# Kernel tuning notes

Hardware: AMD Instinct MI355X
Metric: run time of the kernel (lower is better)

## Reference

```python
import jax, jax.numpy as jnp
import numpy as np

B, S, D_MODEL, H = 2, 2048, 1024, 16
DK = D_MODEL // H
THETA = 10000.0


def setup_inputs() -> dict:
    key = jax.random.key(0)
    ks = jax.random.split(key, 5)
    scale = 0.02  # keep logits in a numerically sane range
    return {
        "x": jax.random.normal(ks[0], (B, S, D_MODEL), jnp.float32),
        "Q_weight": jax.random.normal(ks[1], (D_MODEL, D_MODEL), jnp.float32) * scale,
        "K_weight": jax.random.normal(ks[2], (D_MODEL, D_MODEL), jnp.float32) * scale,
        "V_weight": jax.random.normal(ks[3], (D_MODEL, D_MODEL), jnp.float32) * scale,
        "O_weight": jax.random.normal(ks[4], (D_MODEL, D_MODEL), jnp.float32) * scale,
        "token_positions": jnp.arange(S, dtype=jnp.int32),
    }


def _rope(x, token_positions, theta, d_k):
    # x: [..., seq, d_k]; rotate interleaved even/odd pairs
    inv_freq = 1.0 / theta ** (jnp.arange(0, d_k, 2, dtype=jnp.float32) / d_k)
    ang = token_positions.astype(jnp.float32)[:, None] * inv_freq  # [S, d_k/2]
    cos, sin = jnp.cos(ang), jnp.sin(ang)
    x0, x1 = x[..., 0::2], x[..., 1::2]
    y0 = x0 * cos - x1 * sin
    y1 = x0 * sin + x1 * cos
    return jnp.stack([y0, y1], axis=-1).reshape(x.shape)


def _mhsa(x, Qw, Kw, Vw, Ow, token_positions):
    b, s, d = x.shape
    qw = Qw.reshape(H, DK, d)
    kw = Kw.reshape(H, DK, d)
    vw = Vw.reshape(H, DK, d)
    q = jnp.einsum('hki,bsi->bhsk', qw, x)
    k = jnp.einsum('hki,bsi->bhsk', kw, x)
    v = jnp.einsum('hvi,bsi->bhsv', vw, x)
    q = _rope(q, token_positions, THETA, DK)
    k = _rope(k, token_positions, THETA, DK)
    scores = jnp.einsum('bhnd,bhmd->bhnm', q, k) / jnp.sqrt(jnp.float32(DK))
    causal = jnp.tril(jnp.ones((s, s), dtype=bool))
    scores = jnp.where(causal, scores, -jnp.inf)
    attn = jax.nn.softmax(scores, axis=-1)
    o = jnp.einsum('bhnm,bhmv->bhnv', attn, v)  # [B,H,S,DV]
    o = jnp.transpose(o, (0, 2, 1, 3)).reshape(b, s, H * DK)
    return jnp.einsum('dv,bsv->bsd', Ow, o)


def reference(x, Q_weight, K_weight, V_weight, O_weight, token_positions):
    return _mhsa(x, Q_weight, K_weight, V_weight, O_weight, token_positions)
```

## Files before the change

kernel.cpp:

```cpp
#include <hip/hip_runtime.h>

#define NB 2
#define NS 2048
#define NDM 1024
#define NH 16
#define NDK 64

typedef unsigned int u32;
typedef u32 u32x4 __attribute__((ext_vector_type(4)));
typedef float f32x4 __attribute__((ext_vector_type(4)));
typedef float f32x2 __attribute__((ext_vector_type(2)));
typedef __bf16 bf16x8 __attribute__((ext_vector_type(8)));
typedef __bf16 bf16x4 __attribute__((ext_vector_type(4)));
typedef __bf16 bf16x2 __attribute__((ext_vector_type(2)));

#define QSCALE 0.18033688011112042f
#define EXP2F(x) __builtin_amdgcn_exp2f(x)

__device__ __forceinline__ void gload_lds16(const __bf16* g, __bf16* l) {
    __builtin_amdgcn_global_load_lds(
        (const __attribute__((address_space(1))) unsigned int*)(g),
        (__attribute__((address_space(3))) unsigned int*)(l), 16, 0, 0);
}

__global__ __launch_bounds__(256) void cvt_f32_bf16(const float* __restrict__ src,
                                                    __bf16* __restrict__ dst, int n4) {
    int i = blockIdx.x * blockDim.x + threadIdx.x;
    if (i >= n4) return;
    f32x4 v = *(const f32x4*)(src + (size_t)i * 4);
    bf16x4 o;
    o[0] = (__bf16)v[0]; o[1] = (__bf16)v[1]; o[2] = (__bf16)v[2]; o[3] = (__bf16)v[3];
    *(bf16x4*)(dst + (size_t)i * 4) = o;
}

__global__ __launch_bounds__(256) void cvt_weights(const float* __restrict__ q,
                                                   const float* __restrict__ k,
                                                   const float* __restrict__ v,
                                                   const float* __restrict__ o,
                                                   __bf16* __restrict__ wqkv,
                                                   __bf16* __restrict__ owb) {
    const int seg = blockIdx.y;
    const float* src = (seg == 0) ? q : (seg == 1) ? k : (seg == 2) ? v : o;
    __bf16* dst = (seg == 3) ? owb : wqkv + (size_t)seg * 1024 * 1024;
    const int i = blockIdx.x * 256 + threadIdx.x;
    f32x4 vv = *(const f32x4*)(src + (size_t)i * 4);
    bf16x4 ov;
    ov[0] = (__bf16)vv[0]; ov[1] = (__bf16)vv[1]; ov[2] = (__bf16)vv[2]; ov[3] = (__bf16)vv[3];
    *(bf16x4*)(dst + (size_t)i * 4) = ov;
}

__global__ __launch_bounds__(512, 2) void gemm256(const __bf16* __restrict__ A,
                                                  const __bf16* __restrict__ Bt,
                                                  __bf16* __restrict__ C,
                                                  int K, int lda, int ldb, int ldc, int nbx) {
    __shared__ __bf16 As[2][256 * 64];
    __shared__ __bf16 Bs[2][256 * 64];
    const int tid = threadIdx.x;
    const int lane = tid & 63, w = tid >> 6;
    const int wm = w >> 2, wn = w & 3;
    const int l15 = lane & 15, lg = lane >> 4;
    int bid = blockIdx.x;
    const int cpx = gridDim.x >> 3;
    bid = (bid & 7) * cpx + (bid >> 3);
    const int m0 = (bid / nbx) * 256, n0 = (bid % nbx) * 256;
    const int srow = w * 8 + (lane >> 3);
    const int csw = ((lane & 7) ^ (srow & 7)) * 8;

    f32x4 acc[8][4];
    const f32x4 z = {0.f, 0.f, 0.f, 0.f};
#pragma unroll
    for (int i = 0; i < 8; ++i)
#pragma unroll
        for (int jx = 0; jx < 4; ++jx) acc[i][jx] = z;

    auto stage = [&](int buf, int k0) {
#pragma unroll
        for (int ps = 0; ps < 4; ++ps) {
            const int r = ps * 64 + srow;
            gload_lds16(&A[(size_t)(m0 + r) * lda + k0 + csw], &As[buf][(ps * 64 + w * 8) * 64]);
        }
#pragma unroll
        for (int ps = 0; ps < 4; ++ps) {
            const int r = ps * 64 + srow;
            gload_lds16(&Bt[(size_t)(n0 + r) * ldb + k0 + csw], &Bs[buf][(ps * 64 + w * 8) * 64]);
        }
    };

    stage(0, 0);
    int cur = 0;
    for (int k0 = 0; k0 < K; k0 += 64) {
        if (k0 + 64 < K) {
            stage(cur ^ 1, k0 + 64);
            asm volatile("s_waitcnt vmcnt(8)" ::: "memory");
        } else {
            asm volatile("s_waitcnt vmcnt(0)" ::: "memory");
        }
        __builtin_amdgcn_s_barrier();
        __builtin_amdgcn_sched_barrier(0);
        bf16x8 bfr[4][2];
#pragma unroll
        for (int n = 0; n < 4; ++n)
#pragma unroll
            for (int kc = 0; kc < 2; ++kc) {
                const int rb = wn * 64 + n * 16 + l15;
                bfr[n][kc] = *(const bf16x8*)&Bs[cur][rb * 64 + ((kc * 32 + lg * 8) ^ ((rb & 7) << 3))];
            }
#pragma unroll
        for (int mr = 0; mr < 8; ++mr) {
            bf16x8 af[2];
#pragma unroll
            for (int kc = 0; kc < 2; ++kc) {
                const int ra = wm * 128 + mr * 16 + l15;
                af[kc] = *(const bf16x8*)&As[cur][ra * 64 + ((kc * 32 + lg * 8) ^ ((ra & 7) << 3))];
            }
#pragma unroll
            for (int n = 0; n < 4; ++n)
#pragma unroll
                for (int kc = 0; kc < 2; ++kc)
                    acc[mr][n] = __builtin_amdgcn_mfma_f32_16x16x32_bf16(af[kc], bfr[n][kc], acc[mr][n], 0, 0, 0);
        }
        asm volatile("s_waitcnt lgkmcnt(0)" ::: "memory");
        __builtin_amdgcn_s_barrier();
        __builtin_amdgcn_sched_barrier(0);
        cur ^= 1;
    }
#pragma unroll
    for (int mr = 0; mr < 8; ++mr)
#pragma unroll
        for (int n = 0; n < 4; ++n)
#pragma unroll
            for (int j = 0; j < 4; ++j) {
                const int row = m0 + wm * 128 + mr * 16 + lg * 4 + j;
                const int col = n0 + wn * 64 + n * 16 + l15;
                C[(size_t)row * ldc + col] = (__bf16)acc[mr][n][j];
            }
}

template <typename TOUT>
__global__ __launch_bounds__(256) void gemm_bt128(const __bf16* __restrict__ A,
                                                  const __bf16* __restrict__ Bt,
                                                  TOUT* __restrict__ C,
                                                  int K, int lda, int ldb, int ldc) {
    __shared__ __bf16 As[2][128 * 64];
    __shared__ __bf16 Bs[2][128 * 64];
    const int tid = threadIdx.x;
    const int lane = tid & 63, w = tid >> 6;
    const int wr = w >> 1, wc = w & 1;
    const int l15 = lane & 15, lg = lane >> 4;
    const int m0 = blockIdx.y * 128, n0 = blockIdx.x * 128;
    const int crow = lane >> 3;
    const int csw = ((lane & 7) ^ crow) * 8;

    f32x4 acc[4][4];
    const f32x4 z = {0.f, 0.f, 0.f, 0.f};
#pragma unroll
    for (int i = 0; i < 4; ++i)
#pragma unroll
        for (int jx = 0; jx < 4; ++jx) acc[i][jx] = z;

    auto stage = [&](int buf, int k0) {
#pragma unroll
        for (int ch = 0; ch < 4; ++ch) {
            const int cid = w * 4 + ch;
            const int ra = cid * 8 + crow;
            gload_lds16(&A[(size_t)(m0 + ra) * lda + k0 + csw], &As[buf][cid * 512]);
            gload_lds16(&Bt[(size_t)(n0 + ra) * ldb + k0 + csw], &Bs[buf][cid * 512]);
        }
    };

    stage(0, 0);
    int cur = 0;
    for (int k0 = 0; k0 < K; k0 += 64) {
        if (k0 + 64 < K) {
            stage(cur ^ 1, k0 + 64);
            asm volatile("s_waitcnt vmcnt(8)" ::: "memory");
        } else {
            asm volatile("s_waitcnt vmcnt(0)" ::: "memory");
        }
        __builtin_amdgcn_s_barrier();
        __builtin_amdgcn_sched_barrier(0);
#pragma unroll
        for (int kc = 0; kc < 2; ++kc) {
            bf16x8 af[4], bfv[4];
#pragma unroll
            for (int i = 0; i < 4; ++i) {
                const int ra = wr * 64 + i * 16 + l15;
                const int rb = wc * 64 + i * 16 + l15;
                af[i]  = *(const bf16x8*)&As[cur][ra * 64 + ((kc * 32 + lg * 8) ^ ((ra & 7) << 3))];
                bfv[i] = *(const bf16x8*)&Bs[cur][rb * 64 + ((kc * 32 + lg * 8) ^ ((rb & 7) << 3))];
            }
#pragma unroll
            for (int sm = 0; sm < 4; ++sm)
#pragma unroll
                for (int sn = 0; sn < 4; ++sn)
                    acc[sm][sn] = __builtin_amdgcn_mfma_f32_16x16x32_bf16(af[sm], bfv[sn], acc[sm][sn], 0, 0, 0);
        }
        asm volatile("s_waitcnt lgkmcnt(0)" ::: "memory");
        __builtin_amdgcn_s_barrier();
        __builtin_amdgcn_sched_barrier(0);
        cur ^= 1;
    }
#pragma unroll
    for (int sm = 0; sm < 4; ++sm)
#pragma unroll
        for (int sn = 0; sn < 4; ++sn)
#pragma unroll
            for (int j = 0; j < 4; ++j) {
                const int row = m0 + wr * 64 + sm * 16 + lg * 4 + j;
                const int col = n0 + wc * 64 + sn * 16 + l15;
                C[(size_t)row * ldc + col] = (TOUT)acc[sm][sn][j];
            }
}

__global__ __launch_bounds__(512) void rope_kernel(const __bf16* __restrict__ qkv,
                                                   const int* __restrict__ tp,
                                                   __bf16* __restrict__ Qr,
                                                   __bf16* __restrict__ Kr) {
    const int row = blockIdx.x;
    const int s = row & (NS - 1);
    const int b = row >> 11;
    const int t = threadIdx.x;
    const int h = t >> 5, jj = t & 31;
    const float pos = (float)tp[s];
    const float inv = exp2f(-0.41524101186092f * (float)jj);
    const float ang = pos * inv;
    float sn, cs;
    sincosf(ang, &sn, &cs);
    const __bf16* qp = qkv + (size_t)row * 3072 + h * 64 + 2 * jj;
    bf16x2 qv = *(const bf16x2*)qp;
    bf16x2 kv = *(const bf16x2*)(qp + 1024);
    const float q0 = (float)qv[0], q1 = (float)qv[1];
    const float k0 = (float)kv[0], k1 = (float)kv[1];
    const size_t o = ((size_t)(b * NH + h) * NS + s) * 64 + 2 * jj;
    bf16x2 qo, ko;
    qo[0] = (__bf16)((q0 * cs - q1 * sn) * QSCALE);
    qo[1] = (__bf16)((q0 * sn + q1 * cs) * QSCALE);
    ko[0] = (__bf16)(k0 * cs - k1 * sn); ko[1] = (__bf16)(k0 * sn + k1 * cs);
    *(bf16x2*)&Qr[o] = qo;
    *(bf16x2*)&Kr[o] = ko;
}

__global__ __launch_bounds__(256) void vtrans(const __bf16* __restrict__ qkv,
                                              __bf16* __restrict__ Vt) {
    const int bh = blockIdx.y;
    const int s0 = blockIdx.x * 64;
    const int b = bh >> 4, h = bh & 15;
    __shared__ __bf16 tile[64][72];
    const int t = threadIdx.x;
    const int sl = t >> 3, c8 = (t & 7) * 8;
#pragma unroll
    for (int pp = 0; pp < 2; ++pp) {
        const int srow = sl + pp * 32;
        bf16x8 v = *(const bf16x8*)&qkv[(size_t)(b * NS + s0 + srow) * 3072 + 2048 + h * 64 + c8];
        *(bf16x8*)&tile[srow][c8] = v;
    }
    __syncthreads();
    const int d = t >> 2;
#pragma unroll
    for (int pp = 0; pp < 2; ++pp) {
        const int vec = (t & 3) + pp * 4;
        bf16x8 o;
#pragma unroll
        for (int i = 0; i < 8; ++i) o[i] = tile[vec * 8 + i][d];
        *(bf16x8*)&Vt[((size_t)bh * 64 + d) * NS + s0 + vec * 8] = o;
    }
}

__device__ __forceinline__ int kperm(int rt) {
    const int ct = rt >> 4, rr = rt & 15;
    return ((rr >> 2) << 3) + ((ct >> 1) << 5) + ((ct & 1) << 2) + (rr & 3);
}

__global__ __launch_bounds__(256) void attn5(const __bf16* __restrict__ Qr,
                                             const __bf16* __restrict__ Kr,
                                             const __bf16* __restrict__ Vt,
                                             __bf16* __restrict__ O) {
    const int lid = blockIdx.x;
    const int xcd = lid & 7, ix = lid >> 3;
    const int bh = xcd * 4 + (ix & 3);
    const int p  = ix >> 2;
    const int b = bh >> 4, h = bh & 15;
    const int tid = threadIdx.x;
    const int w = tid >> 6, lane = tid & 63;
    const int l15 = lane & 15, lg = lane >> 4;
    const __bf16* Qb = Qr + (size_t)bh * NS * 64;
    const __bf16* Kb = Kr + (size_t)bh * NS * 64;
    const __bf16* Vb = Vt + (size_t)bh * 64 * NS;

    __shared__ __bf16 Ks[2][64 * 64];
    __shared__ __bf16 Vs[2][64 * 64];

    const int rbv[2] = {p * 64 + w * 16, (31 - p) * 64 + w * 16};

    bf16x8 qf[2][2];
#pragma unroll
    for (int rs = 0; rs < 2; ++rs)
#pragma unroll
        for (int kc = 0; kc < 2; ++kc)
            qf[rs][kc] = *(const bf16x8*)(Qb + (size_t)(rbv[rs] + l15) * 64 + kc * 32 + lg * 8);

    f32x4 oacc[2][4];
    const f32x4 z = {0.f, 0.f, 0.f, 0.f};
#pragma unroll
    for (int rs = 0; rs < 2; ++rs)
#pragma unroll
        for (int ct = 0; ct < 4; ++ct) oacc[rs][ct] = z;
    float m[2], lsum[2];
#pragma unroll
    for (int rs = 0; rs < 2; ++rs) { m[rs] = -1e30f; lsum[rs] = 0.f; }

    const int crow = lane >> 3;
    const int cswz = ((lane & 7) ^ crow) * 8;

#pragma unroll
    for (int pp = 0; pp < 2; ++pp) {
        const int ch = w + pp * 4;
        const int rt = ch * 8 + crow;
        gload_lds16(Kb + (size_t)kperm(rt) * 64 + cswz, &Ks[0][ch * 512]);
        gload_lds16(Vb + (size_t)rt * NS + 0 + cswz, &Vs[0][ch * 512]);
    }
    __syncthreads();

    const int nt = 32 - p;
    for (int t = 0; t < nt; ++t) {
        const int cur = t & 1;
        const int kv0 = t << 6;
        if (t + 1 < nt) {
            const int kv1 = kv0 + 64;
#pragma unroll
            for (int pp = 0; pp < 2; ++pp) {
                const int ch = w + pp * 4;
                const int rt = ch * 8 + crow;
                gload_lds16(Kb + (size_t)(kv1 + kperm(rt)) * 64 + cswz, &Ks[cur ^ 1][ch * 512]);
                gload_lds16(Vb + (size_t)rt * NS + kv1 + cswz, &Vs[cur ^ 1][ch * 512]);
            }
        }
        bool act[2];
        act[0] = (kv0 <= rbv[0] + 15);
        act[1] = true;
        f32x4 sc[2][4];
#pragma unroll
        for (int rs = 0; rs < 2; ++rs)
            if (act[rs])
#pragma unroll
                for (int ct = 0; ct < 4; ++ct) sc[rs][ct] = z;
#pragma unroll
        for (int kc = 0; kc < 2; ++kc) {
            bf16x8 kf[4];
#pragma unroll
            for (int ct = 0; ct < 4; ++ct) {
                const int rt = ct * 16 + l15;
                kf[ct] = *(const bf16x8*)&Ks[cur][rt * 64 + ((kc * 32 + lg * 8) ^ ((rt & 7) << 3))];
            }
#pragma unroll
            for (int rs = 0; rs < 2; ++rs)
                if (act[rs])
#pragma unroll
                    for (int ct = 0; ct < 4; ++ct)
                        sc[rs][ct] = __builtin_amdgcn_mfma_f32_16x16x32_bf16(kf[ct], qf[rs][kc], sc[rs][ct], 0, 0, 0);
        }
        bf16x8 pb[2][2];
#pragma unroll
        for (int rs = 0; rs < 2; ++rs) {
            if (!act[rs]) continue;
            const int rbase = rbv[rs];
            const int qrow = rbase + l15;
            const bool needmask = (kv0 + 63 > rbase);
            if (needmask) {
#pragma unroll
                for (int ct = 0; ct < 4; ++ct)
#pragma unroll
                    for (int j = 0; j < 4; ++j) {
                        const int kvg = kv0 + ((ct >> 1) << 5) + lg * 8 + ((ct & 1) << 2) + j;
                        if (kvg > qrow) sc[rs][ct][j] = -1e30f;
                    }
            }
            float t0 = fmaxf(fmaxf(sc[rs][0][0], sc[rs][0][1]), fmaxf(sc[rs][0][2], sc[rs][0][3]));
            float t1 = fmaxf(fmaxf(sc[rs][1][0], sc[rs][1][1]), fmaxf(sc[rs][1][2], sc[rs][1][3]));
            float t2 = fmaxf(fmaxf(sc[rs][2][0], sc[rs][2][1]), fmaxf(sc[rs][2][2], sc[rs][2][3]));
            float t3 = fmaxf(fmaxf(sc[rs][3][0], sc[rs][3][1]), fmaxf(sc[rs][3][2], sc[rs][3][3]));
            float mt = fmaxf(fmaxf(t0, t1), fmaxf(t2, t3));
            mt = fmaxf(mt, __shfl_xor(mt, 16, 64));
            mt = fmaxf(mt, __shfl_xor(mt, 32, 64));
            float alpha = 1.0f;
            if (!__all(mt - m[rs] <= 12.0f)) {
                const float mn = fmaxf(m[rs], mt);
                alpha = EXP2F(m[rs] - mn);
                m[rs] = mn;
#pragma unroll
                for (int ct = 0; ct < 4; ++ct)
#pragma unroll
                    for (int j = 0; j < 4; ++j) oacc[rs][ct][j] *= alpha;
            }
            float ps = 0.f;
#pragma unroll
            for (int ct = 0; ct < 4; ++ct)
#pragma unroll
                for (int j = 0; j < 4; ++j) {
                    const float e = EXP2F(sc[rs][ct][j] - m[rs]);
                    sc[rs][ct][j] = e;
                    ps += e;
                }
            ps += __shfl_xor(ps, 16, 64);
            ps += __shfl_xor(ps, 32, 64);
            lsum[rs] = lsum[rs] * alpha + ps;
#pragma unroll
            for (int kc = 0; kc < 2; ++kc) {
                bf16x8 pk;
                pk[0] = (__bf16)sc[rs][2 * kc][0];     pk[1] = (__bf16)sc[rs][2 * kc][1];
                pk[2] = (__bf16)sc[rs][2 * kc][2];     pk[3] = (__bf16)sc[rs][2 * kc][3];
                pk[4] = (__bf16)sc[rs][2 * kc + 1][0]; pk[5] = (__bf16)sc[rs][2 * kc + 1][1];
                pk[6] = (__bf16)sc[rs][2 * kc + 1][2]; pk[7] = (__bf16)sc[rs][2 * kc + 1][3];
                pb[rs][kc] = pk;
            }
        }
#pragma unroll
        for (int kc = 0; kc < 2; ++kc) {
            bf16x8 vf[4];
#pragma unroll
            for (int ct = 0; ct < 4; ++ct) {
                const int rt = ct * 16 + l15;
                vf[ct] = *(const bf16x8*)&Vs[cur][rt * 64 + ((kc * 32 + lg * 8) ^ ((rt & 7) << 3))];
            }
#pragma unroll
            for (int rs = 0; rs < 2; ++rs) {
                if (!act[rs]) continue;
#pragma unroll
                for (int ct = 0; ct < 4; ++ct)
                    oacc[rs][ct] = __builtin_amdgcn_mfma_f32_16x16x32_bf16(vf[ct], pb[rs][kc], oacc[rs][ct], 0, 0, 0);
            }
        }
        __syncthreads();
    }
#pragma unroll
    for (int rs = 0; rs < 2; ++rs) {
        const float rl = 1.0f / lsum[rs];
        const size_t rowoff = (size_t)(b * NS + rbv[rs] + l15) * NDM + h * 64 + lg * 4;
#pragma unroll
        for (int ct = 0; ct < 4; ++ct) {
            bf16x4 ov;
#pragma unroll
            for (int j = 0; j < 4; ++j) ov[j] = (__bf16)(oacc[rs][ct][j] * rl);
            *(bf16x4*)&O[rowoff + ct * 16] = ov;
        }
    }
}

extern "C" void kernel_launch(void* const* d_in, const int* in_sizes, int n_in,
                              void* d_out, int out_size, void* d_ws, size_t ws_size,
                              hipStream_t stream) {
    const float* x  = (const float*)d_in[0];
    const float* Qw = (const float*)d_in[1];
    const float* Kw = (const float*)d_in[2];
    const float* Vw = (const float*)d_in[3];
    const float* Ow = (const float*)d_in[4];
    const int*   tp = (const int*)d_in[5];
    float* out = (float*)d_out;

    char* ws = (char*)d_ws;
    size_t off = 0;
    auto alloc = [&](size_t bytes) -> void* {
        void* p = ws + off;
        off += (bytes + 255) & ~(size_t)255;
        return p;
    };
    __bf16* xb   = (__bf16*)alloc((size_t)4096 * 1024 * 2);
    __bf16* wqkv = (__bf16*)alloc((size_t)3072 * 1024 * 2);
    __bf16* owb  = (__bf16*)alloc((size_t)1024 * 1024 * 2);
    __bf16* qkv  = (__bf16*)alloc((size_t)4096 * 3072 * 2);
    __bf16* qr   = (__bf16*)alloc((size_t)32 * 2048 * 64 * 2);
    __bf16* kr   = (__bf16*)alloc((size_t)32 * 2048 * 64 * 2);
    __bf16* vt   = (__bf16*)alloc((size_t)32 * 64 * 2048 * 2);
    __bf16* ob   = (__bf16*)alloc((size_t)4096 * 1024 * 2);

    cvt_f32_bf16<<<4096, 256, 0, stream>>>(x, xb, 4096 * 1024 / 4);
    cvt_weights<<<dim3(1024, 4), 256, 0, stream>>>(Qw, Kw, Vw, Ow, wqkv, owb);

    gemm256<<<192, 512, 0, stream>>>(xb, wqkv, qkv, 1024, 1024, 1024, 3072, 12);
    rope_kernel<<<4096, 512, 0, stream>>>(qkv, tp, qr, kr);
    vtrans<<<dim3(NS / 64, NB * NH), 256, 0, stream>>>(qkv, vt);
    attn5<<<dim3(512), 256, 0, stream>>>(qr, kr, vt, ob);
    gemm_bt128<float><<<dim3(1024 / 128, 4096 / 128), 256, 0, stream>>>(
        ob, owb, out, 1024, 1024, 1024, 1024);
}
```

Measured before the change: 124.9 us.

## Precompute RoPE cos/sin table and use finer waitcnt barriers in attention loop

```diff
diff --git a/kernel.cpp b/kernel.cpp
--- a/kernel.cpp
+++ b/kernel.cpp
@@ -47,6 +47,20 @@
     bf16x4 ov;
     ov[0] = (__bf16)vv[0]; ov[1] = (__bf16)vv[1]; ov[2] = (__bf16)vv[2]; ov[3] = (__bf16)vv[3];
     *(bf16x4*)(dst + (size_t)i * 4) = ov;
+}
+
+__global__ __launch_bounds__(256) void rope_table(const int* __restrict__ tp,
+                                                  float* __restrict__ tbl) {
+    const int i = blockIdx.x * 256 + threadIdx.x;
+    if (i >= NS * 32) return;
+    const int s = i >> 5, jj = i & 31;
+    const float pos = (float)tp[s];
+    const float inv = exp2f(-0.41524101186092f * (float)jj);
+    const float ang = pos * inv;
+    float sn, cs;
+    sincosf(ang, &sn, &cs);
+    f32x2 o; o[0] = cs; o[1] = sn;
+    *(f32x2*)&tbl[(size_t)i * 2] = o;
 }
 
 __global__ __launch_bounds__(512, 2) void gemm256(const __bf16* __restrict__ A,
@@ -213,7 +227,7 @@
 }
 
 __global__ __launch_bounds__(512) void rope_kernel(const __bf16* __restrict__ qkv,
-                                                   const int* __restrict__ tp,
+                                                   const float* __restrict__ tbl,
                                                    __bf16* __restrict__ Qr,
                                                    __bf16* __restrict__ Kr) {
     const int row = blockIdx.x;
@@ -221,11 +235,8 @@
     const int b = row >> 11;
     const int t = threadIdx.x;
     const int h = t >> 5, jj = t & 31;
-    const float pos = (float)tp[s];
-    const float inv = exp2f(-0.41524101186092f * (float)jj);
-    const float ang = pos * inv;
-    float sn, cs;
-    sincosf(ang, &sn, &cs);
+    f32x2 cssn = *(const f32x2*)&tbl[((size_t)s * 32 + jj) * 2];
+    const float cs = cssn[0], sn = cssn[1];
     const __bf16* qp = qkv + (size_t)row * 3072 + h * 64 + 2 * jj;
     bf16x2 qv = *(const bf16x2*)qp;
     bf16x2 kv = *(const bf16x2*)(qp + 1024);
@@ -312,29 +323,29 @@
     const int crow = lane >> 3;
     const int cswz = ((lane & 7) ^ crow) * 8;
 
-#pragma unroll
-    for (int pp = 0; pp < 2; ++pp) {
-        const int ch = w + pp * 4;
-        const int rt = ch * 8 + crow;
-        gload_lds16(Kb + (size_t)kperm(rt) * 64 + cswz, &Ks[0][ch * 512]);
-        gload_lds16(Vb + (size_t)rt * NS + 0 + cswz, &Vs[0][ch * 512]);
-    }
-    __syncthreads();
-
+    auto stage = [&](int buf, int kv) {
+#pragma unroll
+        for (int pp = 0; pp < 2; ++pp) {
+            const int ch = w + pp * 4;
+            const int rt = ch * 8 + crow;
+            gload_lds16(Kb + (size_t)(kv + kperm(rt)) * 64 + cswz, &Ks[buf][ch * 512]);
+            gload_lds16(Vb + (size_t)rt * NS + kv + cswz, &Vs[buf][ch * 512]);
+        }
+    };
+
+    stage(0, 0);
     const int nt = 32 - p;
     for (int t = 0; t < nt; ++t) {
         const int cur = t & 1;
         const int kv0 = t << 6;
         if (t + 1 < nt) {
-            const int kv1 = kv0 + 64;
-#pragma unroll
-            for (int pp = 0; pp < 2; ++pp) {
-                const int ch = w + pp * 4;
-                const int rt = ch * 8 + crow;
-                gload_lds16(Kb + (size_t)(kv1 + kperm(rt)) * 64 + cswz, &Ks[cur ^ 1][ch * 512]);
-                gload_lds16(Vb + (size_t)rt * NS + kv1 + cswz, &Vs[cur ^ 1][ch * 512]);
-            }
-        }
+            stage(cur ^ 1, kv0 + 64);
+            asm volatile("s_waitcnt vmcnt(4)" ::: "memory");
+        } else {
+            asm volatile("s_waitcnt vmcnt(0)" ::: "memory");
+        }
+        __builtin_amdgcn_s_barrier();
+        __builtin_amdgcn_sched_barrier(0);
         bool act[2];
         act[0] = (kv0 <= rbv[0] + 15);
         act[1] = true;
@@ -430,7 +441,9 @@
                     oacc[rs][ct] = __builtin_amdgcn_mfma_f32_16x16x32_bf16(vf[ct], pb[rs][kc], oacc[rs][ct], 0, 0, 0);
             }
         }
-        __syncthreads();
+        asm volatile("s_waitcnt lgkmcnt(0)" ::: "memory");
+        __builtin_amdgcn_s_barrier();
+        __builtin_amdgcn_sched_barrier(0);
     }
 #pragma unroll
     for (int rs = 0; rs < 2; ++rs) {
@@ -472,12 +485,14 @@
     __bf16* kr   = (__bf16*)alloc((size_t)32 * 2048 * 64 * 2);
     __bf16* vt   = (__bf16*)alloc((size_t)32 * 64 * 2048 * 2);
     __bf16* ob   = (__bf16*)alloc((size_t)4096 * 1024 * 2);
+    float*  tbl  = (float*)alloc((size_t)NS * 32 * 2 * 4);
 
     cvt_f32_bf16<<<4096, 256, 0, stream>>>(x, xb, 4096 * 1024 / 4);
     cvt_weights<<<dim3(1024, 4), 256, 0, stream>>>(Qw, Kw, Vw, Ow, wqkv, owb);
+    rope_table<<<(NS * 32 + 255) / 256, 256, 0, stream>>>(tp, tbl);
 
     gemm256<<<192, 512, 0, stream>>>(xb, wqkv, qkv, 1024, 1024, 1024, 3072, 12);
-    rope_kernel<<<4096, 512, 0, stream>>>(qkv, tp, qr, kr);
+    rope_kernel<<<4096, 512, 0, stream>>>(qkv, tbl, qr, kr);
     vtrans<<<dim3(NS / 64, NB * NH), 256, 0, stream>>>(qkv, vt);
     attn5<<<dim3(512), 256, 0, stream>>>(qr, kr, vt, ob);
     gemm_bt128<float><<<dim3(1024 / 128, 4096 / 128), 256, 0, stream>>>(
```

Measured after the change: 127.6 us. 2.2% more time.
